# Optimization experiments

Hardware: AMD Instinct MI355X
Metric: run time of the kernel (lower is better)

Reference implementation:

```python
import math
import jax, jax.numpy as jnp
import numpy as np

B, S, D = 2, 2048, 1024
H, DK = 16, 64
HI, DI = 4, 64
TOP_K = 512


def layernorm(x, gamma, beta, eps=1e-5):
    mu = jnp.mean(x, axis=-1, keepdims=True)
    var = jnp.var(x, axis=-1, keepdims=True)
    return (x - mu) * jax.lax.rsqrt(var + eps) * gamma + beta


def setup_inputs() -> dict:
    key = jax.random.key(0)
    ks = jax.random.split(key, 8)
    x = jax.random.normal(ks[0], (B, S, D), dtype=jnp.float32)
    Q = jax.random.normal(ks[1], (B, H, S, DK), dtype=jnp.float32)
    K = jax.random.normal(ks[2], (B, S, DK), dtype=jnp.float32)
    V = jax.random.normal(ks[3], (B, S, DK), dtype=jnp.float32)
    # indexer linear params (stored input-major: y = x @ W + b)
    Wq_idx = jax.random.normal(ks[4], (D, HI * DI), dtype=jnp.float32) * 0.02
    bq_idx = jnp.zeros((HI * DI,), dtype=jnp.float32)
    Wk_idx = jax.random.normal(ks[5], (D, HI * DI), dtype=jnp.float32) * 0.02
    bk_idx = jnp.zeros((HI * DI,), dtype=jnp.float32)
    ln_gamma = jnp.ones((DI,), dtype=jnp.float32)
    ln_beta = jnp.zeros((DI,), dtype=jnp.float32)
    indexer_weights = jnp.ones((HI,), dtype=jnp.float32) * 0.1
    return {"x": x, "Q": Q, "K": K, "V": V,
            "Wq_idx": Wq_idx, "bq_idx": bq_idx,
            "Wk_idx": Wk_idx, "bk_idx": bk_idx,
            "ln_gamma": ln_gamma, "ln_beta": ln_beta,
            "indexer_weights": indexer_weights}


def reference(x, Q, K, V, Wq_idx, bq_idx, Wk_idx, bk_idx, ln_gamma, ln_beta, indexer_weights):
    b, s, _ = x.shape
    h, d_k = Q.shape[1], Q.shape[-1]
    hi = indexer_weights.shape[0]
    di = ln_gamma.shape[0]

    # indexer projections + per-head layernorm
    q_index = layernorm((x @ Wq_idx + bq_idx).reshape(b, s, hi, di), ln_gamma, ln_beta)
    k_index = layernorm((x @ Wk_idx + bk_idx).reshape(b, s, hi, di), ln_gamma, ln_beta)

    # faithful to torch: s axis from k_index, t axis from q_index
    head_scores = jax.nn.relu(jnp.einsum('bshd,bthd->bhst', k_index, q_index))
    index_scores = jnp.einsum('bhst,h->bst', head_scores, indexer_weights)  # (B,S,S)

    top_k = min(TOP_K, s)
    _, top_idx = jax.lax.top_k(index_scores, top_k)  # (B,S,top_k)

    bidx = jnp.arange(b)[:, None, None]
    K_topk = K[bidx, top_idx]  # (B,S,top_k,d_k)
    V_topk = V[bidx, top_idx]  # (B,S,top_k,d_k)

    Qr = jnp.transpose(Q, (0, 2, 1, 3))  # (B,S,H,d_k)
    attn_scores = jnp.einsum('bshd,bstd->bsht', Qr, K_topk) * (1.0 / math.sqrt(d_k))
    attn_weights = jax.nn.softmax(attn_scores, axis=-1)  # dropout omitted (eval)
    attn_output = jnp.einsum('bsht,bstd->bshd', attn_weights, V_topk).reshape(b, s, h * d_k)

    kl_loss = jnp.zeros((), dtype=x.dtype)  # sparse phase: no KL term
    return attn_output, kl_loss
```

## Files before the change

### kernel.cpp

```cpp
#include <hip/hip_runtime.h>
#include <hip/hip_bf16.h>

#define NB 2
#define NS 2048
#define ND 1024
#define NH 16
#define NDK 64
#define NHI 4
#define NDI 64
#define NTOPK 512

typedef unsigned int u32;

typedef __attribute__((ext_vector_type(8))) short bf16x8;
typedef __attribute__((ext_vector_type(4))) short bf16x4;
typedef __attribute__((ext_vector_type(4))) float f32x4;

__device__ __forceinline__ short f2bf(float f) {
    u32 u = __float_as_uint(f);
    u += 0x7fffu + ((u >> 16) & 1u);
    return (short)(u >> 16);
}
__device__ __forceinline__ float bf2f(short h) {
    return __uint_as_float(((u32)(unsigned short)h) << 16);
}
__device__ __forceinline__ float4 fma4(float4 a, float4 b, float4 c) {
    float4 r;
    r.x = fmaf(a.x, b.x, c.x); r.y = fmaf(a.y, b.y, c.y);
    r.z = fmaf(a.z, b.z, c.z); r.w = fmaf(a.w, b.w, c.w);
    return r;
}

#define TR64(dst, addr, OFF) \
    asm volatile("ds_read_b64_tr_b16 %0, %1 offset:" OFF : "=v"(dst) : "v"(addr))

__global__ __launch_bounds__(256) void k0_split(
    const float* __restrict__ K, const float* __restrict__ V,
    short* __restrict__ Khl, short* __restrict__ Vhl)
{
    int e = blockIdx.x*256 + threadIdx.x;
    int row = e >> 6, d = e & 63;
    float kf = K[e], vf = V[e];
    short kh = f2bf(kf), vh = f2bf(vf);
    short kl = f2bf(kf - bf2f(kh)), vl = f2bf(vf - bf2f(vh));
    Khl[(size_t)row*128 + d]      = kh;
    Khl[(size_t)row*128 + 64 + d] = kl;
    Vhl[(size_t)row*128 + d]      = vh;
    Vhl[(size_t)row*128 + 64 + d] = vl;
}

#define ROWS1 8
__global__ __launch_bounds__(256) void k1_proj_ln(
    const float* __restrict__ x, const float* __restrict__ Wq, const float* __restrict__ bq,
    const float* __restrict__ Wk, const float* __restrict__ bk,
    const float* __restrict__ gamma, const float* __restrict__ beta,
    float* __restrict__ q_index, float* __restrict__ k_index)
{
    __shared__ float4 xs4[ROWS1*256];
    float* projf = reinterpret_cast<float*>(xs4);
    const int tid = threadIdx.x;
    const int m = blockIdx.x & 1;
    const int row0 = (blockIdx.x >> 1) * ROWS1;
    const float* __restrict__ W    = m ? Wk : Wq;
    const float* __restrict__ bias = m ? bk : bq;
    const int c = tid;

    {
        const float4* xg = reinterpret_cast<const float4*>(x) + (size_t)row0 * (ND/4);
        #pragma unroll
        for (int i = 0; i < 8; ++i)
            xs4[tid + 256*i] = xg[tid + 256*i];
    }
    __syncthreads();

    float acc[ROWS1];
    const int panel_lo4[3] = {0, 96, 192};
    const int panel_hi4[3] = {96, 192, 256};
    #pragma unroll
    for (int p = 0; p < 3; ++p) {
        float P[ROWS1];
        #pragma unroll
        for (int r = 0; r < ROWS1; ++r) P[r] = 0.f;
        for (int k4 = panel_lo4[p]; k4 < panel_hi4[p]; ++k4) {
            float4 xv[ROWS1];
            #pragma unroll
            for (int r = 0; r < ROWS1; ++r)
                xv[r] = xs4[r*256 + k4];
            #pragma unroll
            for (int kk = 0; kk < 4; ++kk) {
                float wv = W[(size_t)(k4*4 + kk)*256 + c];
                #pragma unroll
                for (int r = 0; r < ROWS1; ++r) {
                    float xs_ = (kk == 0) ? xv[r].x : (kk == 1) ? xv[r].y : (kk == 2) ? xv[r].z : xv[r].w;
                    P[r] = fmaf(xs_, wv, P[r]);
                }
            }
        }
        #pragma unroll
        for (int r = 0; r < ROWS1; ++r) {
            if (p == 0) acc[r] = P[r];
            else        acc[r] = acc[r] + P[r];
        }
    }
    float bv = bias[c];
    __syncthreads();
    #pragma unroll
    for (int r = 0; r < ROWS1; ++r) projf[r*256 + c] = acc[r] + bv;
    __syncthreads();

    if (tid < ROWS1*4) {
        const int r = tid >> 2, hd = tid & 3;
        const float* pp = &projf[r*256 + hd*64];
        float rr[8];
        #pragma unroll
        for (int q8 = 0; q8 < 8; ++q8) rr[q8] = pp[q8];
        #pragma unroll
        for (int i = 8; i < 64; i += 8)
            #pragma unroll
            for (int q8 = 0; q8 < 8; ++q8) rr[q8] += pp[i + q8];
        float ssum = ((rr[0]+rr[1]) + (rr[2]+rr[3])) + ((rr[4]+rr[5]) + (rr[6]+rr[7]));
        float mu = ssum / 64.0f;

        #pragma unroll
        for (int q8 = 0; q8 < 8; ++q8) { float dv = pp[q8] - mu; rr[q8] = dv*dv; }
        #pragma unroll
        for (int i = 8; i < 64; i += 8)
            #pragma unroll
            for (int q8 = 0; q8 < 8; ++q8) { float dv = pp[i+q8] - mu; rr[q8] += dv*dv; }
        float vsum = ((rr[0]+rr[1]) + (rr[2]+rr[3])) + ((rr[4]+rr[5]) + (rr[6]+rr[7]));
        float var = vsum / 64.0f;
        float inv = 1.0f / (float)sqrt((double)(var + 1e-5f));

        float* dst = (m ? k_index : q_index)
                     + ((size_t)(row0 + r)) * (NHI*NDI) + hd*64;
        for (int i = 0; i < 64; ++i) {
            float dv = pp[i] - mu;
            float t = dv * inv;
            t = t * gamma[i];
            t = t + beta[i];
            dst[i] = t;
        }
    }
}

__global__ __launch_bounds__(256) void k2_scores(
    const float* __restrict__ q_index, const float* __restrict__ k_index,
    const float* __restrict__ hw, u32* __restrict__ keys)
{
    __shared__ float As[64*64];
    __shared__ float Bs[64*64];
    const int tid = threadIdx.x;
    const int t0 = blockIdx.x * 64, s0 = blockIdx.y * 64, b = blockIdx.z;
    const int lane = tid & 63;
    const int wv = tid >> 6;

    float fin[16];
    #pragma unroll
    for (int r = 0; r < 16; ++r) fin[r] = 0.f;

    for (int h = 0; h < NHI; ++h) {
        __syncthreads();
        #pragma unroll
        for (int i = 0; i < 8; ++i) {
            int e = tid + 256*i;
            int side = e >> 10;
            int row = (e >> 4) & 63;
            int q4 = e & 15;
            const float* src = (side ? q_index : k_index)
                + (((size_t)b*NS + (side ? t0 : s0) + row)*NHI + h)*NDI + q4*4;
            float4 v = *reinterpret_cast<const float4*>(src);
            float* dstp = (side ? Bs : As) + row*64 + ((q4 ^ (row & 15)) * 4);
            *reinterpret_cast<float4*>(dstp) = v;
        }
        __syncthreads();

        float4 bf[16];
        #pragma unroll
        for (int q4 = 0; q4 < 16; ++q4)
            bf[q4] = *reinterpret_cast<const float4*>(&Bs[lane*64 + ((q4 ^ (lane & 15)) * 4)]);

        float w = hw[h];
        #pragma unroll
        for (int r = 0; r < 16; ++r) {
            const int row = wv*16 + r;
            const float* ap = &As[row*64];
            const int f = row & 15;
            float4 l0 = {0,0,0,0}, l1 = {0,0,0,0}, l2 = {0,0,0,0}, l3 = {0,0,0,0};
            #pragma unroll
            for (int c = 0; c < 4; ++c) {
                float4 a0 = *reinterpret_cast<const float4*>(ap + (((c*4+0) ^ f) * 4));
                float4 a1 = *reinterpret_cast<const float4*>(ap + (((c*4+1) ^ f) * 4));
                float4 a2 = *reinterpret_cast<const float4*>(ap + (((c*4+2) ^ f) * 4));
                float4 a3 = *reinterpret_cast<const float4*>(ap + (((c*4+3) ^ f) * 4));
                l0 = fma4(a0, bf[c*4+0], l0);
                l1 = fma4(a1, bf[c*4+1], l1);
                l2 = fma4(a2, bf[c*4+2], l2);
                l3 = fma4(a3, bf[c*4+3], l3);
            }
            float4 u, v2, t2;
            u.x=l0.x+l2.x; u.y=l0.y+l2.y; u.z=l0.z+l2.z; u.w=l0.w+l2.w;
            v2.x=l1.x+l3.x; v2.y=l1.y+l3.y; v2.z=l1.z+l3.z; v2.w=l1.w+l3.w;
            t2.x=u.x+v2.x; t2.y=u.y+v2.y; t2.z=u.z+v2.z; t2.w=u.w+v2.w;
            float s3a = t2.x + t2.z, s3b = t2.y + t2.w;
            float dot = s3a + s3b;
            fin[r] = fmaf(w, fmaxf(dot, 0.f), fin[r]);
        }
    }
    #pragma unroll
    for (int r = 0; r < 16; ++r)
        keys[((size_t)b*NS + s0 + wv*16 + r)*NS + t0 + lane] = __float_as_uint(fin[r]);
}

__global__ __launch_bounds__(256) void k3_select(
    const u32* __restrict__ keys_g, int* __restrict__ top_idx)
{
    __shared__ u32 hist[256];
    __shared__ u32 scan[256];
    __shared__ u32 sel_byte, sel_above;
    const int tid = threadIdx.x;
    const size_t row = blockIdx.x;
    const u32* src = keys_g + row * NS;

    u32 keys[8];
    #pragma unroll
    for (int i = 0; i < 8; ++i) keys[i] = src[tid*8 + i];

    u32 prefix = 0, kk = NTOPK, total_gt = 0;
    #pragma unroll
    for (int pass = 0; pass < 4; ++pass) {
        const int shift = 24 - pass*8;
        const u32 mask_hi = (pass == 0) ? 0u : (0xFFFFFFFFu << (shift + 8));
        hist[tid] = 0;
        __syncthreads();
        #pragma unroll
        for (int i = 0; i < 8; ++i)
            if (((keys[i] ^ prefix) & mask_hi) == 0u)
                atomicAdd(&hist[(keys[i] >> shift) & 255], 1u);
        __syncthreads();
        if (tid < 64) {
            u32 v0 = hist[tid*4+0], v1 = hist[tid*4+1], v2 = hist[tid*4+2], v3 = hist[tid*4+3];
            u32 s3 = v3, s2 = v2 + s3, s1 = v1 + s2, s0 = v0 + s1;
            u32 suf = s0;
            #pragma unroll
            for (int o = 1; o < 64; o <<= 1) {
                u32 t = __shfl_down(suf, o, 64);
                if (tid + o < 64) suf += t;
            }
            u32 excl = suf - s0;
            hist[tid*4+0] = s0 + excl;
            hist[tid*4+1] = s1 + excl;
            hist[tid*4+2] = s2 + excl;
            hist[tid*4+3] = s3 + excl;
        }
        __syncthreads();
        if (hist[tid] >= kk && (tid == 255 || hist[tid+1] < kk)) {
            sel_byte = (u32)tid;
            sel_above = (tid == 255) ? 0u : hist[tid+1];
        }
        __syncthreads();
        u32 sb = sel_byte, sa = sel_above;
        prefix |= (sb << shift);
        total_gt += sa;
        kk -= sa;
    }

    const u32 T = prefix;
    const u32 needed = NTOPK - total_gt;

    u32 cgt = 0, ceq = 0;
    #pragma unroll
    for (int i = 0; i < 8; ++i) { cgt += (keys[i] > T); ceq += (keys[i] == T); }
    scan[tid] = (cgt << 16) | ceq;
    __syncthreads();
    if (tid < 64) {
        u32 v0 = scan[tid*4+0], v1 = scan[tid*4+1], v2 = scan[tid*4+2], v3 = scan[tid*4+3];
        u32 p0 = v0, p1 = p0 + v1, p2 = p1 + v2, p3 = p2 + v3;
        u32 pre = p3;
        #pragma unroll
        for (int o = 1; o < 64; o <<= 1) {
            u32 t = __shfl_up(pre, o, 64);
            if (tid >= o) pre += t;
        }
        u32 excl = pre - p3;
        scan[tid*4+0] = p0 + excl;
        scan[tid*4+1] = p1 + excl;
        scan[tid*4+2] = p2 + excl;
        scan[tid*4+3] = p3 + excl;
    }
    __syncthreads();
    u32 incl = scan[tid];
    u32 gt_pref = (incl >> 16) - cgt;
    u32 eq_pref = (incl & 0xFFFFu) - ceq;

    int* dst = top_idx + row * NTOPK;
    u32 lgt = 0, leq = 0;
    #pragma unroll
    for (int i = 0; i < 8; ++i) {
        int idx = tid*8 + i;
        if (keys[i] > T) {
            u32 eqsel = eq_pref + leq; if (eqsel > needed) eqsel = needed;
            u32 slot = gt_pref + lgt + eqsel;
            if (slot < NTOPK) dst[slot] = idx;
            lgt++;
        } else if (keys[i] == T) {
            u32 er = eq_pref + leq;
            if (er < needed) {
                u32 slot = gt_pref + lgt + er;
                if (slot < NTOPK) dst[slot] = idx;
            }
            leq++;
        }
    }
}

__global__ __launch_bounds__(256) void k4_attn_mfma(
    const float* __restrict__ Qg, const short* __restrict__ Khl, const short* __restrict__ Vhl,
    const int* __restrict__ top_idx, float* __restrict__ out)
{
    __shared__ short Ph[NTOPK*16];
    __shared__ short Pl[NTOPK*16];
    __shared__ short Vh[64*64];
    __shared__ short Vl[64*64];
    __shared__ float red[2][16][4];
    __shared__ int   idxs[NTOPK];

    const int tid = threadIdx.x;
    const int l = tid & 63, w = tid >> 6;
    const int q = l >> 4, d15 = l & 15;
    const size_t blk = blockIdx.x;
    const int b = (int)(blk >> 11), s = (int)(blk & 2047);

    for (int i = tid; i < NTOPK; i += 256) idxs[i] = top_idx[blk*NTOPK + i];

    bf16x8 qhi[2], qlo[2];
    {
        const float* qp = Qg + (((size_t)b*NH + d15)*NS + s)*NDK + q*8;
        #pragma unroll
        for (int ks = 0; ks < 2; ++ks) {
            float4 f0 = *reinterpret_cast<const float4*>(qp + ks*32);
            float4 f1 = *reinterpret_cast<const float4*>(qp + ks*32 + 4);
            float fv[8] = {f0.x,f0.y,f0.z,f0.w,f1.x,f1.y,f1.z,f1.w};
            #pragma unroll
            for (int jj = 0; jj < 8; ++jj) {
                short hh = f2bf(fv[jj]);
                qhi[ks][jj] = hh;
                qlo[ks][jj] = f2bf(fv[jj] - bf2f(hh));
            }
        }
    }
    __syncthreads();

    f32x4 sacc[8];
    #pragma unroll
    for (int t = 0; t < 8; ++t) sacc[t] = (f32x4){0.f, 0.f, 0.f, 0.f};

    #pragma unroll
    for (int c = 0; c < 4; ++c) {
        #pragma unroll
        for (int t = 0; t < 2; ++t) {
            int key = c*128 + w*32 + t*16 + d15;
            int kidx = idxs[key];
            const short* rowp = Khl + ((size_t)b*NS + kidx)*128;
            int ti = c*2 + t;
            #pragma unroll
            for (int ks = 0; ks < 2; ++ks) {
                bf16x8 kh = *reinterpret_cast<const bf16x8*>(rowp + ks*32 + q*8);
                bf16x8 kl = *reinterpret_cast<const bf16x8*>(rowp + 64 + ks*32 + q*8);
                sacc[ti] = __builtin_amdgcn_mfma_f32_16x16x32_bf16(qhi[ks], kh, sacc[ti], 0, 0, 0);
                sacc[ti] = __builtin_amdgcn_mfma_f32_16x16x32_bf16(qlo[ks], kh, sacc[ti], 0, 0, 0);
                sacc[ti] = __builtin_amdgcn_mfma_f32_16x16x32_bf16(qhi[ks], kl, sacc[ti], 0, 0, 0);
            }
        }
    }

    bf16x8 vreg[4];
    #pragma unroll
    for (int i = 0; i < 4; ++i) {
        int tt = tid + 256*(i & 3);
        int key = (tt >> 3) & 63, jb = tt & 7, part = tt >> 9;
        vreg[i] = *reinterpret_cast<const bf16x8*>(
            Vhl + ((size_t)b*NS + idxs[0*64 + key])*128 + part*64 + jb*8);
    }

    float m[4], inv[4];
    #pragma unroll
    for (int rg = 0; rg < 4; ++rg) {
        float mm = -3.4e38f;
        #pragma unroll
        for (int t = 0; t < 8; ++t) { sacc[t][rg] *= 0.125f; mm = fmaxf(mm, sacc[t][rg]); }
        #pragma unroll
        for (int o = 1; o <= 8; o <<= 1) mm = fmaxf(mm, __shfl_xor(mm, o));
        m[rg] = mm;
    }
    if (d15 == 0) {
        #pragma unroll
        for (int rg = 0; rg < 4; ++rg) red[0][q*4 + rg][w] = m[rg];
    }
    __syncthreads();
    float sum[4];
    #pragma unroll
    for (int rg = 0; rg < 4; ++rg) {
        int hh = q*4 + rg;
        float g = fmaxf(fmaxf(red[0][hh][0], red[0][hh][1]),
                        fmaxf(red[0][hh][2], red[0][hh][3]));
        float ss = 0.f;
        #pragma unroll
        for (int t = 0; t < 8; ++t) { float p = __expf(sacc[t][rg] - g); sacc[t][rg] = p; ss += p; }
        #pragma unroll
        for (int o = 1; o <= 8; o <<= 1) ss += __shfl_xor(ss, o);
        sum[rg] = ss;
    }
    if (d15 == 0) {
        #pragma unroll
        for (int rg = 0; rg < 4; ++rg) red[1][q*4 + rg][w] = sum[rg];
    }
    __syncthreads();
    #pragma unroll
    for (int rg = 0; rg < 4; ++rg) {
        int hh = q*4 + rg;
        inv[rg] = 1.f / (red[1][hh][0] + red[1][hh][1] + red[1][hh][2] + red[1][hh][3]);
    }

    #pragma unroll
    for (int t = 0; t < 8; ++t) {
        int key = (t >> 1)*128 + w*32 + (t & 1)*16 + d15;
        bf16x4 h4, l4;
        #pragma unroll
        for (int rg = 0; rg < 4; ++rg) {
            float p = sacc[t][rg] * inv[rg];
            short ph_ = f2bf(p);
            h4[rg] = ph_;
            l4[rg] = f2bf(p - bf2f(ph_));
        }
        *reinterpret_cast<bf16x4*>(&Ph[key*16 + q*4]) = h4;
        *reinterpret_cast<bf16x4*>(&Pl[key*16 + q*4]) = l4;
    }

    #pragma unroll
    for (int i = 0; i < 4; ++i) {
        int tt = tid + 256*(i & 3);
        int key = (tt >> 3) & 63, jb = tt & 7, part = tt >> 9;
        short* dstp = (part ? Vl : Vh) + key*64 + (((jb*2) ^ ((key & 3) << 2)) * 4);
        *reinterpret_cast<bf16x8*>(dstp) = vreg[i];
    }
    __syncthreads();

    const unsigned phb = (unsigned)(size_t)&Ph[0];
    const unsigned plb = (unsigned)(size_t)&Pl[0];
    const unsigned vhb = (unsigned)(size_t)&Vh[0];
    const unsigned vlb = (unsigned)(size_t)&Vl[0];

    f32x4 oacc = (f32x4){0.f, 0.f, 0.f, 0.f};
    #pragma unroll
    for (int c = 0; c < 8; ++c) {
        if (c < 7) {
            #pragma unroll
            for (int i = 0; i < 4; ++i) {
                int tt = tid + 256*(i & 3);
                int key = (tt >> 3) & 63, jb = tt & 7, part = tt >> 9;
                vreg[i] = *reinterpret_cast<const bf16x8*>(
                    Vhl + ((size_t)b*NS + idxs[(c+1)*64 + key])*128 + part*64 + jb*8);
            }
        }
        #pragma unroll
        for (int ks = 0; ks < 2; ++ks) {
            unsigned pa = phb + (unsigned)((c*64 + ks*32 + 8*q + (d15 >> 2))*32 + (d15 & 3)*8);
            unsigned pla = pa + (plb - phb);
            unsigned va = vhb + (unsigned)((ks*32 + 8*q + (d15 >> 2))*128
                                           + (((w*4 + (d15 & 3)) ^ ((d15 >> 2) << 2)) * 8));
            unsigned vla = va + (vlb - vhb);
            bf16x4 p0, p1, r0, r1, v0, v1, u0, u1;
            TR64(p0, pa,  "0");   TR64(p1, pa,  "128");
            TR64(r0, pla, "0");   TR64(r1, pla, "128");
            TR64(v0, va,  "0");   TR64(v1, va,  "512");
            TR64(u0, vla, "0");   TR64(u1, vla, "512");
            asm volatile("s_waitcnt lgkmcnt(0)" ::: "memory");
            __builtin_amdgcn_sched_barrier(0);
            bf16x8 pH = __builtin_shufflevector(p0, p1, 0,1,2,3,4,5,6,7);
            bf16x8 pL = __builtin_shufflevector(r0, r1, 0,1,2,3,4,5,6,7);
            bf16x8 vH = __builtin_shufflevector(v0, v1, 0,1,2,3,4,5,6,7);
            bf16x8 vL = __builtin_shufflevector(u0, u1, 0,1,2,3,4,5,6,7);
            oacc = __builtin_amdgcn_mfma_f32_16x16x32_bf16(pH, vH, oacc, 0, 0, 0);
            oacc = __builtin_amdgcn_mfma_f32_16x16x32_bf16(pL, vH, oacc, 0, 0, 0);
            oacc = __builtin_amdgcn_mfma_f32_16x16x32_bf16(pH, vL, oacc, 0, 0, 0);
        }
        if (c < 7) {
            __syncthreads();
            #pragma unroll
            for (int i = 0; i < 4; ++i) {
                int tt = tid + 256*(i & 3);
                int key = (tt >> 3) & 63, jb = tt & 7, part = tt >> 9;
                short* dstp = (part ? Vl : Vh) + key*64 + (((jb*2) ^ ((key & 3) << 2)) * 4);
                *reinterpret_cast<bf16x8*>(dstp) = vreg[i];
            }
            __syncthreads();
        }
    }

    #pragma unroll
    for (int rg = 0; rg < 4; ++rg) {
        int hh = q*4 + rg;
        out[((size_t)b*NS + s)*(NH*NDK) + hh*NDK + w*16 + d15] = oacc[rg];
    }
    if (blk == 0 && tid == 0) out[(size_t)NB*NS*NH*NDK] = 0.f;
}

extern "C" void kernel_launch(void* const* d_in, const int* in_sizes, int n_in,
                              void* d_out, int out_size, void* d_ws, size_t ws_size,
                              hipStream_t stream) {
    const float* x     = (const float*)d_in[0];
    const float* Q     = (const float*)d_in[1];
    const float* K     = (const float*)d_in[2];
    const float* V     = (const float*)d_in[3];
    const float* Wq    = (const float*)d_in[4];
    const float* bq    = (const float*)d_in[5];
    const float* Wk    = (const float*)d_in[6];
    const float* bk    = (const float*)d_in[7];
    const float* gamma = (const float*)d_in[8];
    const float* beta  = (const float*)d_in[9];
    const float* hw    = (const float*)d_in[10];
    float* outp = (float*)d_out;

    float* q_index = (float*)d_ws;
    float* k_index = q_index + (size_t)NB*NS*NHI*NDI;
    u32*   keys    = (u32*)(k_index + (size_t)NB*NS*NHI*NDI);
    short* Khl     = (short*)(keys + (size_t)NB*NS*NS);
    short* Vhl     = Khl + (size_t)NB*NS*128;
    int*   top_idx = (int*)d_ws;

    k0_split<<<(NB*NS*NDK)/256, 256, 0, stream>>>(K, V, Khl, Vhl);
    k1_proj_ln<<<(NB*NS/ROWS1)*2, 256, 0, stream>>>(x, Wq, bq, Wk, bk, gamma, beta, q_index, k_index);
    k2_scores<<<dim3(NS/64, NS/64, NB), 256, 0, stream>>>(q_index, k_index, hw, keys);
    k3_select<<<NB*NS, 256, 0, stream>>>(keys, top_idx);
    k4_attn_mfma<<<NB*NS, 256, 0, stream>>>(Q, Khl, Vhl, top_idx, outp);
}
```

Before: 334.3 us.

## Drop LDS staging in projection and score kernels, read operands directly from global

The projection kernel no longer copies the x rows into shared memory. It reads them as float4 straight from global memory, which removes one barrier and the LDS staging. The score kernel drops its shared-memory tiles entirely. Each wave now computes a 32x64 tile, reading the q_index columns per lane and the wave-uniform k_index rows directly from global or cache, with a larger grid tile and a launch-bounds occupancy hint. This removes LDS traffic and barriers but depends on the cache serving repeated and broadcast global loads, and uncoalesced per-lane row reads could cost more than they save.

```diff
diff --git a/kernel.cpp b/kernel.cpp
--- a/kernel.cpp
+++ b/kernel.cpp
@@ -56,22 +56,15 @@
     const float* __restrict__ gamma, const float* __restrict__ beta,
     float* __restrict__ q_index, float* __restrict__ k_index)
 {
-    __shared__ float4 xs4[ROWS1*256];
-    float* projf = reinterpret_cast<float*>(xs4);
+    __shared__ float projf[ROWS1*256];
     const int tid = threadIdx.x;
     const int m = blockIdx.x & 1;
     const int row0 = (blockIdx.x >> 1) * ROWS1;
     const float* __restrict__ W    = m ? Wk : Wq;
     const float* __restrict__ bias = m ? bk : bq;
     const int c = tid;
-
-    {
-        const float4* xg = reinterpret_cast<const float4*>(x) + (size_t)row0 * (ND/4);
-        #pragma unroll
-        for (int i = 0; i < 8; ++i)
-            xs4[tid + 256*i] = xg[tid + 256*i];
-    }
-    __syncthreads();
+    const float4* __restrict__ xg =
+        reinterpret_cast<const float4*>(x) + (size_t)row0 * (ND/4);
 
     float acc[ROWS1];
     const int panel_lo4[3] = {0, 96, 192};
@@ -85,7 +78,7 @@
             float4 xv[ROWS1];
             #pragma unroll
             for (int r = 0; r < ROWS1; ++r)
-                xv[r] = xs4[r*256 + k4];
+                xv[r] = xg[r*256 + k4];
             #pragma unroll
             for (int kk = 0; kk < 4; ++kk) {
                 float wv = W[(size_t)(k4*4 + kk)*256 + c];
@@ -103,7 +96,6 @@
         }
     }
     float bv = bias[c];
-    __syncthreads();
     #pragma unroll
     for (int r = 0; r < ROWS1; ++r) projf[r*256 + c] = acc[r] + bv;
     __syncthreads();
@@ -143,72 +135,63 @@
     }
 }
 
-__global__ __launch_bounds__(256) void k2_scores(
+__global__ __launch_bounds__(256, 4) void k2_scores(
     const float* __restrict__ q_index, const float* __restrict__ k_index,
     const float* __restrict__ hw, u32* __restrict__ keys)
 {
-    __shared__ float As[64*64];
-    __shared__ float Bs[64*64];
-    const int tid = threadIdx.x;
-    const int t0 = blockIdx.x * 64, s0 = blockIdx.y * 64, b = blockIdx.z;
+    const int tid  = threadIdx.x;
     const int lane = tid & 63;
-    const int wv = tid >> 6;
-
-    float fin[16];
-    #pragma unroll
-    for (int r = 0; r < 16; ++r) fin[r] = 0.f;
-
-    for (int h = 0; h < NHI; ++h) {
-        __syncthreads();
-        #pragma unroll
-        for (int i = 0; i < 8; ++i) {
-            int e = tid + 256*i;
-            int side = e >> 10;
-            int row = (e >> 4) & 63;
-            int q4 = e & 15;
-            const float* src = (side ? q_index : k_index)
-                + (((size_t)b*NS + (side ? t0 : s0) + row)*NHI + h)*NDI + q4*4;
-            float4 v = *reinterpret_cast<const float4*>(src);
-            float* dstp = (side ? Bs : As) + row*64 + ((q4 ^ (row & 15)) * 4);
-            *reinterpret_cast<float4*>(dstp) = v;
-        }
-        __syncthreads();
-
-        float4 bf[16];
-        #pragma unroll
-        for (int q4 = 0; q4 < 16; ++q4)
-            bf[q4] = *reinterpret_cast<const float4*>(&Bs[lane*64 + ((q4 ^ (lane & 15)) * 4)]);
-
-        float w = hw[h];
-        #pragma unroll
-        for (int r = 0; r < 16; ++r) {
-            const int row = wv*16 + r;
-            const float* ap = &As[row*64];
-            const int f = row & 15;
-            float4 l0 = {0,0,0,0}, l1 = {0,0,0,0}, l2 = {0,0,0,0}, l3 = {0,0,0,0};
-            #pragma unroll
-            for (int c = 0; c < 4; ++c) {
-                float4 a0 = *reinterpret_cast<const float4*>(ap + (((c*4+0) ^ f) * 4));
-                float4 a1 = *reinterpret_cast<const float4*>(ap + (((c*4+1) ^ f) * 4));
-                float4 a2 = *reinterpret_cast<const float4*>(ap + (((c*4+2) ^ f) * 4));
-                float4 a3 = *reinterpret_cast<const float4*>(ap + (((c*4+3) ^ f) * 4));
-                l0 = fma4(a0, bf[c*4+0], l0);
-                l1 = fma4(a1, bf[c*4+1], l1);
-                l2 = fma4(a2, bf[c*4+2], l2);
-                l3 = fma4(a3, bf[c*4+3], l3);
-            }
-            float4 u, v2, t2;
-            u.x=l0.x+l2.x; u.y=l0.y+l2.y; u.z=l0.z+l2.z; u.w=l0.w+l2.w;
-            v2.x=l1.x+l3.x; v2.y=l1.y+l3.y; v2.z=l1.z+l3.z; v2.w=l1.w+l3.w;
-            t2.x=u.x+v2.x; t2.y=u.y+v2.y; t2.z=u.z+v2.z; t2.w=u.w+v2.w;
-            float s3a = t2.x + t2.z, s3b = t2.y + t2.w;
-            float dot = s3a + s3b;
-            fin[r] = fmaf(w, fmaxf(dot, 0.f), fin[r]);
-        }
-    }
-    #pragma unroll
-    for (int r = 0; r < 16; ++r)
-        keys[((size_t)b*NS + s0 + wv*16 + r)*NS + t0 + lane] = __float_as_uint(fin[r]);
+    const int w    = tid >> 6;
+    const int b    = blockIdx.z;
+    const int t0   = blockIdx.x * 128 + (w >> 1) * 64;
+    const int s0   = blockIdx.y * 64  + (w & 1) * 32;
+    const int tcol = t0 + lane;
+
+    const float* __restrict__ bbase = q_index + ((size_t)b*NS + tcol)*(NHI*NDI);
+
+    #pragma unroll
+    for (int half = 0; half < 2; ++half) {
+        const int r0 = s0 + half*16;
+        float fin[16];
+        #pragma unroll
+        for (int r = 0; r < 16; ++r) fin[r] = 0.f;
+
+        for (int h = 0; h < NHI; ++h) {
+            float4 bf[16];
+            #pragma unroll
+            for (int q4 = 0; q4 < 16; ++q4)
+                bf[q4] = *reinterpret_cast<const float4*>(bbase + h*NDI + q4*4);
+            float wgt = hw[h];
+
+            #pragma unroll
+            for (int r = 0; r < 16; ++r) {
+                const float* __restrict__ ap =
+                    k_index + (((size_t)b*NS + r0 + r)*NHI + h)*NDI;
+                float4 l0 = {0,0,0,0}, l1 = {0,0,0,0}, l2 = {0,0,0,0}, l3 = {0,0,0,0};
+                #pragma unroll
+                for (int cc = 0; cc < 4; ++cc) {
+                    float4 a0 = *reinterpret_cast<const float4*>(ap + cc*16 + 0);
+                    float4 a1 = *reinterpret_cast<const float4*>(ap + cc*16 + 4);
+                    float4 a2 = *reinterpret_cast<const float4*>(ap + cc*16 + 8);
+                    float4 a3 = *reinterpret_cast<const float4*>(ap + cc*16 + 12);
+                    l0 = fma4(a0, bf[cc*4+0], l0);
+                    l1 = fma4(a1, bf[cc*4+1], l1);
+                    l2 = fma4(a2, bf[cc*4+2], l2);
+                    l3 = fma4(a3, bf[cc*4+3], l3);
+                }
+                float4 u, v2, t2;
+                u.x=l0.x+l2.x; u.y=l0.y+l2.y; u.z=l0.z+l2.z; u.w=l0.w+l2.w;
+                v2.x=l1.x+l3.x; v2.y=l1.y+l3.y; v2.z=l1.z+l3.z; v2.w=l1.w+l3.w;
+                t2.x=u.x+v2.x; t2.y=u.y+v2.y; t2.z=u.z+v2.z; t2.w=u.w+v2.w;
+                float s3a = t2.x + t2.z, s3b = t2.y + t2.w;
+                float dot = s3a + s3b;
+                fin[r] = fmaf(wgt, fmaxf(dot, 0.f), fin[r]);
+            }
+        }
+        #pragma unroll
+        for (int r = 0; r < 16; ++r)
+            keys[((size_t)b*NS + r0 + r)*NS + tcol] = __float_as_uint(fin[r]);
+    }
 }
 
 __global__ __launch_bounds__(256) void k3_select(
@@ -530,7 +513,7 @@
 
     k0_split<<<(NB*NS*NDK)/256, 256, 0, stream>>>(K, V, Khl, Vhl);
     k1_proj_ln<<<(NB*NS/ROWS1)*2, 256, 0, stream>>>(x, Wq, bq, Wk, bk, gamma, beta, q_index, k_index);
-    k2_scores<<<dim3(NS/64, NS/64, NB), 256, 0, stream>>>(q_index, k_index, hw, keys);
+    k2_scores<<<dim3(NS/128, NS/64, NB), 256, 0, stream>>>(q_index, k_index, hw, keys);
     k3_select<<<NB*NS, 256, 0, stream>>>(keys, top_idx);
     k4_attn_mfma<<<NB*NS, 256, 0, stream>>>(Q, Khl, Vhl, top_idx, outp);
 }
```

After: 688.7 us. 2.06x slower.

## Read x directly from global in projection and broadcast A via readlane

Applied to the files above, without the earlier changes.

The projection kernel stops staging x rows in shared memory and loads them straight from global memory, removing a shared buffer and a barrier. In the score kernel, each lane loads one element of the A row and the 64 values are broadcast with readlane instead of every lane reading the whole row from LDS. This targets LDS bandwidth and occupancy, but adds repeated global loads of x and many scalar-register broadcast instructions.

```diff
diff --git a/kernel.cpp b/kernel.cpp
--- a/kernel.cpp
+++ b/kernel.cpp
@@ -29,6 +29,9 @@
     r.x = fmaf(a.x, b.x, c.x); r.y = fmaf(a.y, b.y, c.y);
     r.z = fmaf(a.z, b.z, c.z); r.w = fmaf(a.w, b.w, c.w);
     return r;
+}
+__device__ __forceinline__ float bcast_lane(float v, int k) {
+    return __int_as_float(__builtin_amdgcn_readlane(__float_as_int(v), k));
 }
 
 #define TR64(dst, addr, OFF) \
@@ -56,22 +59,15 @@
     const float* __restrict__ gamma, const float* __restrict__ beta,
     float* __restrict__ q_index, float* __restrict__ k_index)
 {
-    __shared__ float4 xs4[ROWS1*256];
-    float* projf = reinterpret_cast<float*>(xs4);
+    __shared__ float projf[ROWS1*256];
     const int tid = threadIdx.x;
     const int m = blockIdx.x & 1;
     const int row0 = (blockIdx.x >> 1) * ROWS1;
     const float* __restrict__ W    = m ? Wk : Wq;
     const float* __restrict__ bias = m ? bk : bq;
     const int c = tid;
-
-    {
-        const float4* xg = reinterpret_cast<const float4*>(x) + (size_t)row0 * (ND/4);
-        #pragma unroll
-        for (int i = 0; i < 8; ++i)
-            xs4[tid + 256*i] = xg[tid + 256*i];
-    }
-    __syncthreads();
+    const float4* __restrict__ xg =
+        reinterpret_cast<const float4*>(x) + (size_t)row0 * (ND/4);
 
     float acc[ROWS1];
     const int panel_lo4[3] = {0, 96, 192};
@@ -85,7 +81,7 @@
             float4 xv[ROWS1];
             #pragma unroll
             for (int r = 0; r < ROWS1; ++r)
-                xv[r] = xs4[r*256 + k4];
+                xv[r] = xg[r*256 + k4];
             #pragma unroll
             for (int kk = 0; kk < 4; ++kk) {
                 float wv = W[(size_t)(k4*4 + kk)*256 + c];
@@ -103,7 +99,6 @@
         }
     }
     float bv = bias[c];
-    __syncthreads();
     #pragma unroll
     for (int r = 0; r < ROWS1; ++r) projf[r*256 + c] = acc[r] + bv;
     __syncthreads();
@@ -183,25 +178,34 @@
         #pragma unroll
         for (int r = 0; r < 16; ++r) {
             const int row = wv*16 + r;
-            const float* ap = &As[row*64];
             const int f = row & 15;
-            float4 l0 = {0,0,0,0}, l1 = {0,0,0,0}, l2 = {0,0,0,0}, l3 = {0,0,0,0};
+            float av = As[row*64 + ((((lane >> 2) ^ f) << 2) | (lane & 3))];
+            float acc16[16];
+            #pragma unroll
+            for (int j = 0; j < 16; ++j) acc16[j] = 0.f;
             #pragma unroll
             for (int c = 0; c < 4; ++c) {
-                float4 a0 = *reinterpret_cast<const float4*>(ap + (((c*4+0) ^ f) * 4));
-                float4 a1 = *reinterpret_cast<const float4*>(ap + (((c*4+1) ^ f) * 4));
-                float4 a2 = *reinterpret_cast<const float4*>(ap + (((c*4+2) ^ f) * 4));
-                float4 a3 = *reinterpret_cast<const float4*>(ap + (((c*4+3) ^ f) * 4));
-                l0 = fma4(a0, bf[c*4+0], l0);
-                l1 = fma4(a1, bf[c*4+1], l1);
-                l2 = fma4(a2, bf[c*4+2], l2);
-                l3 = fma4(a3, bf[c*4+3], l3);
-            }
-            float4 u, v2, t2;
-            u.x=l0.x+l2.x; u.y=l0.y+l2.y; u.z=l0.z+l2.z; u.w=l0.w+l2.w;
-            v2.x=l1.x+l3.x; v2.y=l1.y+l3.y; v2.z=l1.z+l3.z; v2.w=l1.w+l3.w;
-            t2.x=u.x+v2.x; t2.y=u.y+v2.y; t2.z=u.z+v2.z; t2.w=u.w+v2.w;
-            float s3a = t2.x + t2.z, s3b = t2.y + t2.w;
+                #pragma unroll
+                for (int i = 0; i < 4; ++i) {
+                    float bx = bf[c*4+i].x, by = bf[c*4+i].y,
+                          bz = bf[c*4+i].z, bw = bf[c*4+i].w;
+                    int kbase = c*16 + i*4;
+                    acc16[i*4+0] = fmaf(bcast_lane(av, kbase+0), bx, acc16[i*4+0]);
+                    acc16[i*4+1] = fmaf(bcast_lane(av, kbase+1), by, acc16[i*4+1]);
+                    acc16[i*4+2] = fmaf(bcast_lane(av, kbase+2), bz, acc16[i*4+2]);
+                    acc16[i*4+3] = fmaf(bcast_lane(av, kbase+3), bw, acc16[i*4+3]);
+                }
+            }
+            float u0 = acc16[0]  + acc16[8];
+            float u1 = acc16[1]  + acc16[9];
+            float u2 = acc16[2]  + acc16[10];
+            float u3 = acc16[3]  + acc16[11];
+            float v0 = acc16[4]  + acc16[12];
+            float v1 = acc16[5]  + acc16[13];
+            float v2_ = acc16[6] + acc16[14];
+            float v3 = acc16[7]  + acc16[15];
+            float tx = u0 + v0, ty = u1 + v1, tz = u2 + v2_, tw = u3 + v3;
+            float s3a = tx + tz, s3b = ty + tw;
             float dot = s3a + s3b;
             fin[r] = fmaf(w, fmaxf(dot, 0.f), fin[r]);
         }
```

Measured after the change: 486.1 us. +45.4%, slower.
